# Kernel tuning notes

Hardware: AMD Instinct MI355X
Metric: run time of the kernel (lower is better)

Reference implementation:

```python
import jax, jax.numpy as jnp
import numpy as np

# Dims (match init_kwargs config)
D_L, D_A, D_V = 300, 74, 35
DH_L, DH_A, DH_V = 512, 256, 256
MEM = 512
H_MLP = 1024          # h_att1 = h_att2 = h_gamma1 = h_gamma2 = h_out
T, N = 64, 1024
TOTAL_H = DH_L + DH_A + DH_V          # 1024
ATT_IN = 2 * TOTAL_H                  # 2048 (windowsize=2)
GAMMA_IN = ATT_IN + MEM               # 2560
FINAL = TOTAL_H + MEM                 # 1536


def setup_inputs() -> dict:
    key = jax.random.key(0)
    ks = iter(jax.random.split(key, 64))
    def p(shape):
        return jax.random.normal(next(ks), shape, jnp.float32) * 0.05
    inp = {
        "x": jax.random.normal(next(ks), (T, N, D_L + D_A + D_V), jnp.float32),
        "h_l_prior": jnp.zeros((N, DH_L), jnp.float32),
        "h_a_prior": jnp.zeros((N, DH_A), jnp.float32),
        "h_v_prior": jnp.zeros((N, DH_V), jnp.float32),
        "mem_prior": jnp.zeros((N, MEM), jnp.float32),
        # LSTMCell params (torch layout: W_ih [4H, In], gate order i,f,g,o)
        "W_ih_l": p((4 * DH_L, D_L)), "W_hh_l": p((4 * DH_L, DH_L)),
        "b_ih_l": p((4 * DH_L,)), "b_hh_l": p((4 * DH_L,)),
        "W_ih_a": p((4 * DH_A, D_A)), "W_hh_a": p((4 * DH_A, DH_A)),
        "b_ih_a": p((4 * DH_A,)), "b_hh_a": p((4 * DH_A,)),
        "W_ih_v": p((4 * DH_V, D_V)), "W_hh_v": p((4 * DH_V, DH_V)),
        "b_ih_v": p((4 * DH_V,)), "b_hh_v": p((4 * DH_V,)),
        # attention / gamma / out MLPs (torch Linear: weight [out, in])
        "att1_w1": p((H_MLP, ATT_IN)), "att1_b1": p((H_MLP,)),
        "att1_w2": p((ATT_IN, H_MLP)), "att1_b2": p((ATT_IN,)),
        "att2_w1": p((H_MLP, ATT_IN)), "att2_b1": p((H_MLP,)),
        "att2_w2": p((MEM, H_MLP)), "att2_b2": p((MEM,)),
        "g1_w1": p((H_MLP, GAMMA_IN)), "g1_b1": p((H_MLP,)),
        "g1_w2": p((MEM, H_MLP)), "g1_b2": p((MEM,)),
        "g2_w1": p((H_MLP, GAMMA_IN)), "g2_b1": p((H_MLP,)),
        "g2_w2": p((MEM, H_MLP)), "g2_b2": p((MEM,)),
        "out_w1": p((H_MLP, FINAL)), "out_b1": p((H_MLP,)),
        "out_w2": p((1, H_MLP)), "out_b2": p((1,)),
    }
    return inp


def _lstm_cell(xt, h, c, Wih, Whh, bih, bhh):
    g = xt @ Wih.T + bih + h @ Whh.T + bhh
    i, f, gg, o = jnp.split(g, 4, axis=1)
    c2 = jax.nn.sigmoid(f) * c + jax.nn.sigmoid(i) * jnp.tanh(gg)
    h2 = jax.nn.sigmoid(o) * jnp.tanh(c2)
    return h2, c2


def _mlp2(z, w1, b1, w2, b2):
    # fc2(relu(fc1(z))); dropout is identity at inference
    return jax.nn.relu(z @ w1.T + b1) @ w2.T + b2


def reference(x, h_l_prior, h_a_prior, h_v_prior, mem_prior,
              W_ih_l, W_hh_l, b_ih_l, b_hh_l,
              W_ih_a, W_hh_a, b_ih_a, b_hh_a,
              W_ih_v, W_hh_v, b_ih_v, b_hh_v,
              att1_w1, att1_b1, att1_w2, att1_b2,
              att2_w1, att2_b1, att2_w2, att2_b2,
              g1_w1, g1_b1, g1_w2, g1_b2,
              g2_w1, g2_b1, g2_w2, g2_b2,
              out_w1, out_b1, out_w2, out_b2):
    n = x.shape[1]
    x_l = x[:, :, :D_L]
    x_a = x[:, :, D_L:D_L + D_A]
    x_v = x[:, :, D_L + D_A:]
    # states are re-initialized to zeros (priors unused, as in original forward)
    z = lambda d: jnp.zeros((n, d), x.dtype)
    carry = (z(DH_L), z(DH_L), z(DH_A), z(DH_A), z(DH_V), z(DH_V), z(MEM))

    def step(carry, xs):
        h_l, c_l, h_a, c_a, h_v, c_v, mem = carry
        xl, xa, xv = xs
        nh_l, nc_l = _lstm_cell(xl, h_l, c_l, W_ih_l, W_hh_l, b_ih_l, b_hh_l)
        nh_a, nc_a = _lstm_cell(xa, h_a, c_a, W_ih_a, W_hh_a, b_ih_a, b_hh_a)
        nh_v, nc_v = _lstm_cell(xv, h_v, c_v, W_ih_v, W_hh_v, b_ih_v, b_hh_v)
        # cStar = [prev_cs, new_cs]  -> [n, 2*TOTAL_H]
        cStar = jnp.concatenate([c_l, c_a, c_v, nc_l, nc_a, nc_v], axis=1)
        att = jax.nn.softmax(_mlp2(cStar, att1_w1, att1_b1, att1_w2, att1_b2), axis=1)
        attended = att * cStar
        cHat = jnp.tanh(_mlp2(attended, att2_w1, att2_b1, att2_w2, att2_b2))
        both = jnp.concatenate([attended, mem], axis=1)
        gamma1 = jax.nn.sigmoid(_mlp2(both, g1_w1, g1_b1, g1_w2, g1_b2))
        gamma2 = jax.nn.sigmoid(_mlp2(both, g2_w1, g2_b1, g2_w2, g2_b2))
        mem2 = gamma1 * mem + gamma2 * cHat
        return (nh_l, nc_l, nh_a, nc_a, nh_v, nc_v, mem2), None

    (h_l, c_l, h_a, c_a, h_v, c_v, mem), _ = jax.lax.scan(step, carry, (x_l, x_a, x_v))
    last_hs = jnp.concatenate([h_l, h_a, h_v, mem], axis=1)  # [n, FINAL]
    return _mlp2(last_hs, out_w1, out_b1, out_w2, out_b2)     # [n, 1]
```

## Files before the change

kernel.cpp:

```cpp
#include <hip/hip_runtime.h>
#include <hip/hip_bf16.h>

typedef unsigned short u16;
typedef unsigned int   u32;
typedef __attribute__((ext_vector_type(8))) short s16x8;
typedef __attribute__((ext_vector_type(4))) float f32x4;

#define NB   1024
#define TT   64
#define DXL  300
#define DXA  74
#define DXV  35
#define DX   (DXL+DXA+DXV)
#define DHL  512
#define DHA  256
#define DHV  256
#define TOTH 1024
#define MEMD 512
#define HMLP 1024
#define ATTIN 2048
#define GAMIN 2560
#define PXL  320
#define PXA  128
#define PXV  64

__device__ __forceinline__ u16 f2b(float f) {
    union { float f; u32 u; } x; x.f = f;
    u32 r = x.u + 0x7fffu + ((x.u >> 16) & 1u);
    return (u16)(r >> 16);
}

__device__ __forceinline__ void gload_lds16(const void* g, void* l) {
    __builtin_amdgcn_global_load_lds(
        (const __attribute__((address_space(1))) unsigned int*)g,
        (__attribute__((address_space(3))) unsigned int*)l,
        16, 0, 0);
}

struct GP {
    const u16* A0; const u16* A1; const u16* W0; const u16* W1;
    const float* b0; const float* b1; void* C;
    int lda0, K0, lda1, K1, ldw0, ldw1, ldc, act, outbf, bStart, gx;
};

__global__ __launch_bounds__(256) void gemm_group(GP p0, GP p1, GP p2,
                                                  GP p3, GP p4, GP p5)
{
    __shared__ u16 As[2][64 * 64];
    __shared__ u16 Bs[2][64 * 64];
    GP p;
    {
        int bx = blockIdx.x;
        if      (bx >= p5.bStart) p = p5;
        else if (bx >= p4.bStart) p = p4;
        else if (bx >= p3.bStart) p = p3;
        else if (bx >= p2.bStart) p = p2;
        else if (bx >= p1.bStart) p = p1;
        else                      p = p0;
    }
    const int tid  = threadIdx.x;
    const int wid  = tid >> 6;
    const int lane = tid & 63;
    const int local = blockIdx.x - p.bStart;
    const int by  = local / p.gx;
    const int bm  = by * 64;
    const int bn  = (local - by * p.gx) * 64;
    const int wr = wid >> 1, wc = wid & 1;
    const int nt = (p.K0 + p.K1) >> 6;
    const int e0 = wid * 2 * 64 + lane;

    auto stage = [&](int t, int buf) {
        int k0 = t << 6;
        const u16 *Ap, *Wp; int ldA, ldW, ka;
        if (k0 < p.K0) { Ap = p.A0; ldA = p.lda0; ka = k0;        Wp = p.W0; ldW = p.ldw0; }
        else           { Ap = p.A1; ldA = p.lda1; ka = k0 - p.K0; Wp = p.W1; ldW = p.ldw1; }
        #pragma unroll
        for (int i = 0; i < 2; ++i) {
            int e   = e0 + i * 64;
            int row = e >> 3;
            int c   = (e & 7) ^ (row & 7);
            gload_lds16(Ap + (size_t)(bm + row) * ldA + ka + c * 8,
                        (char*)&As[buf][0] + (wid * 2 + i) * 1024);
            gload_lds16(Wp + (size_t)(bn + row) * ldW + ka + c * 8,
                        (char*)&Bs[buf][0] + (wid * 2 + i) * 1024);
        }
    };

    f32x4 acc[2][2] = {};
    stage(0, 0);
    __syncthreads();

    for (int t = 0; t < nt; ++t) {
        if (t + 1 < nt) stage(t + 1, (t + 1) & 1);
        const char* Ab = (const char*)&As[t & 1][0];
        const char* Bb = (const char*)&Bs[t & 1][0];
        #pragma unroll
        for (int ks = 0; ks < 2; ++ks) {
            s16x8 af[2], bf[2];
            const int ca = ks * 4 + (lane >> 4);
            #pragma unroll
            for (int f = 0; f < 2; ++f) {
                int ra = wr * 32 + f * 16 + (lane & 15);
                af[f] = *(const s16x8*)(Ab + ra * 128 + ((ca ^ (ra & 7))) * 16);
                int rb = wc * 32 + f * 16 + (lane & 15);
                bf[f] = *(const s16x8*)(Bb + rb * 128 + ((ca ^ (rb & 7))) * 16);
            }
            #pragma unroll
            for (int fi = 0; fi < 2; ++fi)
                #pragma unroll
                for (int fj = 0; fj < 2; ++fj)
                    acc[fi][fj] = __builtin_amdgcn_mfma_f32_16x16x32_bf16(
                        af[fi], bf[fj], acc[fi][fj], 0, 0, 0);
        }
        __syncthreads();
    }

    #pragma unroll
    for (int fi = 0; fi < 2; ++fi)
        #pragma unroll
        for (int fj = 0; fj < 2; ++fj) {
            int col = bn + wc * 32 + fj * 16 + (lane & 15);
            float bia = p.b0[col];
            if (p.b1) bia += p.b1[col];
            #pragma unroll
            for (int r4 = 0; r4 < 4; ++r4) {
                int row = bm + wr * 32 + fi * 16 + (lane >> 4) * 4 + r4;
                float v = acc[fi][fj][r4] + bia;
                if (p.act == 1)      v = fmaxf(v, 0.f);
                else if (p.act == 2) v = 1.f / (1.f + __expf(-v));
                else if (p.act == 3) v = tanhf(v);
                if (p.outbf) ((u16*)p.C)[(size_t)row * p.ldc + col] = f2b(v);
                else         ((float*)p.C)[(size_t)row * p.ldc + col] = v;
            }
        }
}

__device__ __forceinline__ void lstm_elem(
    const float* __restrict__ gl, const float* __restrict__ ga,
    const float* __restrict__ gv, const float* __restrict__ cs_prev,
    float* __restrict__ cs_new, u16* __restrict__ cs_new_b,
    u16* __restrict__ hs_new_b, int idx)
{
    int n = idx >> 10, u = idx & 1023;
    const float* g; int dh, gu;
    if (u < DHL)            { g = gl; dh = DHL; gu = u; }
    else if (u < DHL + DHA) { g = ga; dh = DHA; gu = u - DHL; }
    else                    { g = gv; dh = DHV; gu = u - DHL - DHA; }
    const float* grow = g + (size_t)n * 4 * dh;
    float gi = grow[gu], gf = grow[dh + gu], gg = grow[2 * dh + gu], go = grow[3 * dh + gu];
    float c  = cs_prev[idx];
    float si = 1.f / (1.f + __expf(-gi));
    float sf = 1.f / (1.f + __expf(-gf));
    float so = 1.f / (1.f + __expf(-go));
    float c2 = sf * c + si * tanhf(gg);
    float h2 = so * tanhf(c2);
    cs_new[idx]   = c2;
    cs_new_b[idx] = f2b(c2);
    hs_new_b[idx] = f2b(h2);
}

__device__ __forceinline__ void xcvt_elem(
    const float* __restrict__ X, int t, int n, int u,
    u16* __restrict__ xl, u16* __restrict__ xa, u16* __restrict__ xv)
{
    const float* row = X + ((size_t)t * NB + n) * DX;
    if (u < PXL)            xl[n * PXL + u] = f2b(u < DXL ? row[u] : 0.f);
    else if (u < PXL + PXA) { int q = u - PXL;       xa[n * PXA + q] = f2b(q < DXA ? row[DXL + q] : 0.f); }
    else                    { int q = u - PXL - PXA; xv[n * PXV + q] = f2b(q < DXV ? row[DXL + DXA + q] : 0.f); }
}

__global__ void lstm_pointwise(const float* __restrict__ gl,
                               const float* __restrict__ ga,
                               const float* __restrict__ gv,
                               const float* __restrict__ cs_prev,
                               float* __restrict__ cs_new,
                               u16* __restrict__ cs_new_b,
                               u16* __restrict__ hs_new_b,
                               const float* __restrict__ X, int tnext,
                               u16* __restrict__ xl, u16* __restrict__ xa,
                               u16* __restrict__ xv)
{
    int idx = blockIdx.x * blockDim.x + threadIdx.x;
    if (idx >= NB * TOTH) return;
    lstm_elem(gl, ga, gv, cs_prev, cs_new, cs_new_b, hs_new_b, idx);
    int n = idx >> 10, u = idx & 1023;
    if (tnext < TT && u < 512) xcvt_elem(X, tnext, n, u, xl, xa, xv);
}

__global__ __launch_bounds__(256) void fused_mid(
    const float* __restrict__ logits,
    const float* __restrict__ csP,
    const float* __restrict__ csN,
    u16* __restrict__ attended_b,
    int do_mem,
    float* __restrict__ memb, u16* __restrict__ membb,
    const float* __restrict__ g1, const float* __restrict__ g2,
    const float* __restrict__ chat,
    int do_pw,
    const float* __restrict__ gl, const float* __restrict__ ga,
    const float* __restrict__ gv,
    float* __restrict__ pw_cs_new,
    u16* __restrict__ pw_cs_new_b,
    u16* __restrict__ pw_hs_new_b,
    const float* __restrict__ X, int tnext,
    u16* __restrict__ xl, u16* __restrict__ xa, u16* __restrict__ xv)
{
    int n = blockIdx.x;
    int tid = threadIdx.x, lane = tid & 63, wid = tid >> 6;

    if (do_mem) {
        for (int k = tid; k < MEMD; k += 256) {
            size_t i = (size_t)n * MEMD + k;
            float v = g1[i] * memb[i] + g2[i] * chat[i];
            memb[i]  = v;
            membb[i] = f2b(v);
        }
    }

    const float* z = logits + (size_t)n * ATTIN;
    __shared__ float sred[4];

    float m = -1e30f;
    for (int k = tid; k < ATTIN; k += 256) m = fmaxf(m, z[k]);
    #pragma unroll
    for (int off = 1; off < 64; off <<= 1) m = fmaxf(m, __shfl_xor(m, off));
    if (lane == 0) sred[wid] = m;
    __syncthreads();
    m = fmaxf(fmaxf(sred[0], sred[1]), fmaxf(sred[2], sred[3]));
    __syncthreads();

    float s = 0.f;
    for (int k = tid; k < ATTIN; k += 256) s += __expf(z[k] - m);
    #pragma unroll
    for (int off = 1; off < 64; off <<= 1) s += __shfl_xor(s, off);
    if (lane == 0) sred[wid] = s;
    __syncthreads();
    s = sred[0] + sred[1] + sred[2] + sred[3];
    float inv = 1.f / s;

    for (int k = tid; k < ATTIN; k += 256) {
        float cs = (k < TOTH) ? csP[(size_t)n * TOTH + k]
                              : csN[(size_t)n * TOTH + (k - TOTH)];
        attended_b[(size_t)n * ATTIN + k] = f2b(__expf(z[k] - m) * inv * cs);
    }

    if (do_pw) {
        __syncthreads();
        #pragma unroll
        for (int j = 0; j < 4; ++j) {
            int u = tid + j * 256;
            lstm_elem(gl, ga, gv, csN, pw_cs_new, pw_cs_new_b, pw_hs_new_b,
                      n * 1024 + u);
        }
        if (tnext < TT) {
            #pragma unroll
            for (int j = 0; j < 2; ++j) {
                int u = tid + j * 256;
                xcvt_elem(X, tnext, n, u, xl, xa, xv);
            }
        }
    }
}

__global__ void mem_update(float* __restrict__ memb,
                           u16* __restrict__ memb_b,
                           const float* __restrict__ g1,
                           const float* __restrict__ g2,
                           const float* __restrict__ chat)
{
    int idx = blockIdx.x * blockDim.x + threadIdx.x;
    if (idx >= NB * MEMD) return;
    float v = g1[idx] * memb[idx] + g2[idx] * chat[idx];
    memb[idx]   = v;
    memb_b[idx] = f2b(v);
}

__global__ __launch_bounds__(256) void out_dot(const float* __restrict__ hid,
                                               const float* __restrict__ w2,
                                               const float* __restrict__ b2,
                                               float* __restrict__ out)
{
    int wid = threadIdx.x >> 6, lane = threadIdx.x & 63;
    int n = blockIdx.x * 4 + wid;
    if (n >= NB) return;
    const float* h = hid + (size_t)n * HMLP;
    float s = 0.f;
    for (int k = lane; k < HMLP; k += 64) s += h[k] * w2[k];
    #pragma unroll
    for (int off = 1; off < 64; off <<= 1) s += __shfl_xor(s, off);
    if (lane == 0) out[n] = s + b2[0];
}

__global__ void cvt_x(const float* __restrict__ X,
                      u16* __restrict__ xl, u16* __restrict__ xa, u16* __restrict__ xv,
                      int t)
{
    int idx = blockIdx.x * blockDim.x + threadIdx.x;
    if (idx >= NB * 512) return;
    xcvt_elem(X, t, idx >> 9, idx & 511, xl, xa, xv);
}

__global__ void concat2(const float* __restrict__ a, const float* __restrict__ b,
                        float* __restrict__ d)
{
    int i = blockIdx.x * 256 + threadIdx.x;
    if (i < 1024)      d[i] = a[i];
    else if (i < 2048) d[i] = b[i - 1024];
}

#define NWC 15
struct WDesc { const float* src; u16* dst; int rows, ksrc, kdst, bstart; };
struct WPack { WDesc d[NWC]; };

__global__ __launch_bounds__(256) void wcvt_all(WPack wp)
{
    int bx = blockIdx.x;
    int di = 0;
    #pragma unroll
    for (int i = 1; i < NWC; ++i) if (bx >= wp.d[i].bstart) di = i;
    WDesc d = wp.d[di];
    int n = d.rows * d.kdst;
    int base = (bx - d.bstart) * 2048 + threadIdx.x;
    if (d.ksrc == d.kdst) {
        #pragma unroll
        for (int j = 0; j < 8; ++j) {
            int idx = base + j * 256;
            if (idx < n) d.dst[idx] = f2b(d.src[idx]);
        }
    } else {
        #pragma unroll
        for (int j = 0; j < 8; ++j) {
            int idx = base + j * 256;
            if (idx < n) {
                int r = idx / d.kdst, c = idx - r * d.kdst;
                d.dst[idx] = f2b(c < d.ksrc ? d.src[(size_t)r * d.ksrc + c] : 0.f);
            }
        }
    }
}

__global__ void fill0(u32* __restrict__ p, int n)
{
    int i = blockIdx.x * blockDim.x + threadIdx.x;
    if (i < n) p[i] = 0u;
}

static GP mkgp(const u16* A0, int lda0, int K0, const u16* A1, int lda1, int K1,
               const u16* W0, int ldw0, const u16* W1, int ldw1,
               const float* b0, const float* b1, void* C, int ldc,
               int Nout, int act, int outbf)
{
    GP p;
    p.A0 = A0; p.A1 = A1; p.W0 = W0; p.W1 = W1; p.b0 = b0; p.b1 = b1; p.C = C;
    p.lda0 = lda0; p.K0 = K0; p.lda1 = lda1; p.K1 = K1;
    p.ldw0 = ldw0; p.ldw1 = ldw1; p.ldc = ldc; p.act = act; p.outbf = outbf;
    p.bStart = 0; p.gx = Nout / 64;
    return p;
}

static void launch_group(hipStream_t s, GP* p, int np)
{
    int total = 0;
    for (int i = 0; i < np; ++i) { p[i].bStart = total; total += p[i].gx * 16; }
    GP dummy = {};
    dummy.bStart = 0x7fffffff;
    GP a1 = (np > 1) ? p[1] : dummy;
    GP a2 = (np > 2) ? p[2] : dummy;
    GP a3 = (np > 3) ? p[3] : dummy;
    GP a4 = (np > 4) ? p[4] : dummy;
    GP a5 = (np > 5) ? p[5] : dummy;
    gemm_group<<<dim3(total), 256, 0, s>>>(p[0], a1, a2, a3, a4, a5);
}

extern "C" void kernel_launch(void* const* d_in, const int* in_sizes, int n_in,
                              void* d_out, int out_size, void* d_ws, size_t ws_size,
                              hipStream_t stream)
{
    const float* X     = (const float*)d_in[0];
    const float* Wih_l = (const float*)d_in[5];
    const float* Whh_l = (const float*)d_in[6];
    const float* bih_l = (const float*)d_in[7];
    const float* bhh_l = (const float*)d_in[8];
    const float* Wih_a = (const float*)d_in[9];
    const float* Whh_a = (const float*)d_in[10];
    const float* bih_a = (const float*)d_in[11];
    const float* bhh_a = (const float*)d_in[12];
    const float* Wih_v = (const float*)d_in[13];
    const float* Whh_v = (const float*)d_in[14];
    const float* bih_v = (const float*)d_in[15];
    const float* bhh_v = (const float*)d_in[16];
    const float* a1w1  = (const float*)d_in[17];
    const float* a1b1  = (const float*)d_in[18];
    const float* a1w2  = (const float*)d_in[19];
    const float* a1b2  = (const float*)d_in[20];
    const float* a2w1  = (const float*)d_in[21];
    const float* a2b1  = (const float*)d_in[22];
    const float* a2w2  = (const float*)d_in[23];
    const float* a2b2  = (const float*)d_in[24];
    const float* g1w1  = (const float*)d_in[25];
    const float* g1b1  = (const float*)d_in[26];
    const float* g1w2  = (const float*)d_in[27];
    const float* g1b2  = (const float*)d_in[28];
    const float* g2w1  = (const float*)d_in[29];
    const float* g2b1  = (const float*)d_in[30];
    const float* g2w2  = (const float*)d_in[31];
    const float* g2b2  = (const float*)d_in[32];
    const float* ow1   = (const float*)d_in[33];
    const float* ob1   = (const float*)d_in[34];
    const float* ow2   = (const float*)d_in[35];
    const float* ob2   = (const float*)d_in[36];
    float* out = (float*)d_out;

    char* wsp = (char*)d_ws;
    auto take = [&](size_t bytes) -> char* {
        char* r = wsp; wsp += (bytes + 255) & ~(size_t)255; return r;
    };
    float* cs0  = (float*)take((size_t)NB * TOTH * 4);
    float* cs1  = (float*)take((size_t)NB * TOTH * 4);
    float* memb = (float*)take((size_t)NB * MEMD * 4);
    float* gl   = (float*)take((size_t)NB * 2048 * 4);
    float* ga   = (float*)take((size_t)NB * 1024 * 4);
    float* gv   = (float*)take((size_t)NB * 1024 * 4);
    float* lgts = (float*)take((size_t)NB * ATTIN * 4);
    float* chat = (float*)take((size_t)NB * MEMD * 4);
    float* gm1  = (float*)take((size_t)NB * MEMD * 4);
    float* gm2  = (float*)take((size_t)NB * MEMD * 4);
    float* hout = (float*)take((size_t)NB * HMLP * 4);
    float* cb2  = (float*)take((size_t)2048 * 4);
    u16* hs0b  = (u16*)take((size_t)NB * TOTH * 2);
    u16* hs1b  = (u16*)take((size_t)NB * TOTH * 2);
    u16* cs0b  = (u16*)take((size_t)NB * TOTH * 2);
    u16* cs1b  = (u16*)take((size_t)NB * TOTH * 2);
    u16* membb = (u16*)take((size_t)NB * MEMD * 2);
    u16* xlb   = (u16*)take((size_t)NB * PXL * 2);
    u16* xab   = (u16*)take((size_t)NB * PXA * 2);
    u16* xvb   = (u16*)take((size_t)NB * PXV * 2);
    u16* hid1b = (u16*)take((size_t)NB * HMLP * 2);
    u16* hcat  = (u16*)take((size_t)NB * 3072 * 2);
    u16* attdb = (u16*)take((size_t)NB * ATTIN * 2);
    u16* wihlb = (u16*)take((size_t)2048 * PXL * 2);
    u16* whhlb = (u16*)take((size_t)2048 * DHL * 2);
    u16* wihab = (u16*)take((size_t)1024 * PXA * 2);
    u16* whhab = (u16*)take((size_t)1024 * DHA * 2);
    u16* wihvb = (u16*)take((size_t)1024 * PXV * 2);
    u16* whhvb = (u16*)take((size_t)1024 * DHV * 2);
    u16* a1w1b = (u16*)take((size_t)HMLP * ATTIN * 2);
    u16* a1w2b = (u16*)take((size_t)ATTIN * HMLP * 2);
    u16* a2w1b = (u16*)take((size_t)HMLP * ATTIN * 2);
    u16* g12w1b= (u16*)take((size_t)2048 * GAMIN * 2);
    u16* a2w2b = (u16*)take((size_t)MEMD * HMLP * 2);
    u16* g1w2b = (u16*)take((size_t)MEMD * HMLP * 2);
    u16* g2w2b = (u16*)take((size_t)MEMD * HMLP * 2);
    u16* ow1b  = (u16*)take((size_t)HMLP * 1536 * 2);

    {
        int nf = NB * (TOTH * 2 + MEMD);
        fill0<<<(nf + 255) / 256, 256, 0, stream>>>((u32*)cs0, nf);
        int nb = NB * (TOTH * 4 + MEMD) / 2;
        fill0<<<(nb + 255) / 256, 256, 0, stream>>>((u32*)hs0b, nb);
    }
    {
        WPack wp;
        const float* src[NWC] = { Wih_l, Whh_l, Wih_a, Whh_a, Wih_v, Whh_v,
                                  a1w1, a1w2, a2w1, g1w1, g2w1,
                                  a2w2, g1w2, g2w2, ow1 };
        u16* dst[NWC] = { wihlb, whhlb, wihab, whhab, wihvb, whhvb,
                          a1w1b, a1w2b, a2w1b, g12w1b, g12w1b + (size_t)1024 * GAMIN,
                          a2w2b, g1w2b, g2w2b, ow1b };
        int rows[NWC] = { 2048, 2048, 1024, 1024, 1024, 1024,
                          HMLP, ATTIN, HMLP, 1024, 1024,
                          MEMD, MEMD, MEMD, HMLP };
        int ksrc[NWC] = { DXL, DHL, DXA, DHA, DXV, DHV,
                          ATTIN, HMLP, ATTIN, GAMIN, GAMIN,
                          HMLP, HMLP, HMLP, 1536 };
        int kdst[NWC] = { PXL, DHL, PXA, DHA, PXV, DHV,
                          ATTIN, HMLP, ATTIN, GAMIN, GAMIN,
                          HMLP, HMLP, HMLP, 1536 };
        int total = 0;
        for (int i = 0; i < NWC; ++i) {
            wp.d[i].src = src[i]; wp.d[i].dst = dst[i];
            wp.d[i].rows = rows[i]; wp.d[i].ksrc = ksrc[i]; wp.d[i].kdst = kdst[i];
            wp.d[i].bstart = total;
            total += (rows[i] * kdst[i] + 2047) / 2048;
        }
        wcvt_all<<<total, 256, 0, stream>>>(wp);
    }
    concat2<<<8, 256, 0, stream>>>(g1b1, g2b1, cb2);
    cvt_x<<<(NB * 512 + 255) / 256, 256, 0, stream>>>(X, xlb, xab, xvb, 0);

    float* csf[2] = { cs0, cs1 };
    u16*   csb[2] = { cs0b, cs1b };
    u16*   hsb[2] = { hs0b, hs1b };

    {
        GP ps[3] = {
            mkgp(xlb, PXL, PXL, hsb[0], TOTH, DHL,
                 wihlb, PXL, whhlb, DHL, bih_l, bhh_l, gl, 2048, 2048, 0, 0),
            mkgp(xab, PXA, PXA, hsb[0] + DHL, TOTH, DHA,
                 wihab, PXA, whhab, DHA, bih_a, bhh_a, ga, 1024, 1024, 0, 0),
            mkgp(xvb, PXV, PXV, hsb[0] + DHL + DHA, TOTH, DHV,
                 wihvb, PXV, whhvb, DHV, bih_v, bhh_v, gv, 1024, 1024, 0, 0) };
        launch_group(stream, ps, 3);
    }
    lstm_pointwise<<<(NB * TOTH + 255) / 256, 256, 0, stream>>>(
        gl, ga, gv, csf[0], csf[1], csb[1], hsb[1], X, 1, xlb, xab, xvb);
    {
        GP ps[4] = {
            mkgp(csb[0], TOTH, TOTH, csb[1], TOTH, TOTH,
                 a1w1b, ATTIN, a1w1b + TOTH, ATTIN, a1b1, nullptr,
                 hid1b, HMLP, HMLP, 1, 1),
            mkgp(xlb, PXL, PXL, hsb[1], TOTH, DHL,
                 wihlb, PXL, whhlb, DHL, bih_l, bhh_l, gl, 2048, 2048, 0, 0),
            mkgp(xab, PXA, PXA, hsb[1] + DHL, TOTH, DHA,
                 wihab, PXA, whhab, DHA, bih_a, bhh_a, ga, 1024, 1024, 0, 0),
            mkgp(xvb, PXV, PXV, hsb[1] + DHL + DHA, TOTH, DHV,
                 wihvb, PXV, whhvb, DHV, bih_v, bhh_v, gv, 1024, 1024, 0, 0) };
        launch_group(stream, ps, 4);
    }
    {
        GP ps[1] = { mkgp(hid1b, HMLP, HMLP, nullptr, 0, 0,
                          a1w2b, HMLP, nullptr, 0, a1b2, nullptr,
                          lgts, ATTIN, ATTIN, 0, 0) };
        launch_group(stream, ps, 1);
    }

    for (int t = 0; t < TT; ++t) {
        fused_mid<<<NB, 256, 0, stream>>>(
            lgts, csf[t & 1], csf[(t + 1) & 1], attdb,
            t > 0 ? 1 : 0, memb, membb, gm1, gm2, chat,
            t < TT - 1 ? 1 : 0, gl, ga, gv,
            csf[t & 1], csb[t & 1], hsb[t & 1],
            X, t + 2, xlb, xab, xvb);

        {
            GP ps[6]; int np = 0;
            ps[np++] = mkgp(attdb, ATTIN, ATTIN, membb, MEMD, MEMD,
                            g12w1b, GAMIN, g12w1b + ATTIN, GAMIN, cb2, nullptr,
                            hcat + 1024, 3072, 2048, 1, 1);
            ps[np++] = mkgp(attdb, ATTIN, ATTIN, nullptr, 0, 0,
                            a2w1b, ATTIN, nullptr, 0, a2b1, nullptr,
                            hcat, 3072, 1024, 1, 1);
            if (t < TT - 1)
                ps[np++] = mkgp(csb[(t + 1) & 1], TOTH, TOTH, csb[t & 1], TOTH, TOTH,
                                a1w1b, ATTIN, a1w1b + TOTH, ATTIN, a1b1, nullptr,
                                hid1b, HMLP, HMLP, 1, 1);
            if (t < TT - 2) {
                ps[np++] = mkgp(xlb, PXL, PXL, hsb[t & 1], TOTH, DHL,
                                wihlb, PXL, whhlb, DHL, bih_l, bhh_l, gl, 2048, 2048, 0, 0);
                ps[np++] = mkgp(xab, PXA, PXA, hsb[t & 1] + DHL, TOTH, DHA,
                                wihab, PXA, whhab, DHA, bih_a, bhh_a, ga, 1024, 1024, 0, 0);
                ps[np++] = mkgp(xvb, PXV, PXV, hsb[t & 1] + DHL + DHA, TOTH, DHV,
                                wihvb, PXV, whhvb, DHV, bih_v, bhh_v, gv, 1024, 1024, 0, 0);
            }
            launch_group(stream, ps, np);
        }

        {
            GP ps[4]; int np = 0;
            if (t < TT - 1)
                ps[np++] = mkgp(hid1b, HMLP, HMLP, nullptr, 0, 0,
                                a1w2b, HMLP, nullptr, 0, a1b2, nullptr,
                                lgts, ATTIN, ATTIN, 0, 0);
            ps[np++] = mkgp(hcat, 3072, HMLP, nullptr, 0, 0,
                            a2w2b, HMLP, nullptr, 0, a2b2, nullptr, chat, MEMD, MEMD, 3, 0);
            ps[np++] = mkgp(hcat + 1024, 3072, HMLP, nullptr, 0, 0,
                            g1w2b, HMLP, nullptr, 0, g1b2, nullptr, gm1, MEMD, MEMD, 2, 0);
            ps[np++] = mkgp(hcat + 2048, 3072, HMLP, nullptr, 0, 0,
                            g2w2b, HMLP, nullptr, 0, g2b2, nullptr, gm2, MEMD, MEMD, 2, 0);
            launch_group(stream, ps, np);
        }
    }

    mem_update<<<(NB * MEMD + 255) / 256, 256, 0, stream>>>(memb, membb, gm1, gm2, chat);
    {
        GP ps[1] = { mkgp(hsb[0], TOTH, TOTH, membb, MEMD, MEMD,
                          ow1b, 1536, ow1b + TOTH, 1536, ob1, nullptr,
                          hout, HMLP, HMLP, 1, 0) };
        launch_group(stream, ps, 1);
    }
    out_dot<<<NB / 4, 256, 0, stream>>>(hout, ow2, ob2, out);
}
```

Measured before the change: 5.255 ms.

## Prepack weights into MFMA fragment order and load B directly from global

Weights are converted once into a tile- and fragment-major bf16 layout, so each lane reads its B-operand fragment with a single contiguous 16-byte global load. This removes the B shared-memory tile, its async copy and the LDS reads, halving LDS use per block, and launch bounds now request 8 blocks per CU. The cost is that B operands are no longer shared through LDS across waves (each wave fetches its own half from L2/global), and the global load latency sits directly in the MFMA loop with no software prefetch.

```diff
diff --git a/kernel.cpp b/kernel.cpp
--- a/kernel.cpp
+++ b/kernel.cpp
@@ -38,16 +38,15 @@
 }
 
 struct GP {
-    const u16* A0; const u16* A1; const u16* W0; const u16* W1;
+    const u16* A0; const u16* A1; const u16* Wpk;
     const float* b0; const float* b1; void* C;
-    int lda0, K0, lda1, K1, ldw0, ldw1, ldc, act, outbf, bStart, gx;
+    int lda0, K0, lda1, K1, ldc, act, outbf, bStart, gx;
 };
 
-__global__ __launch_bounds__(256) void gemm_group(GP p0, GP p1, GP p2,
-                                                  GP p3, GP p4, GP p5)
+__global__ __launch_bounds__(256, 8) void gemm_group(GP p0, GP p1, GP p2,
+                                                     GP p3, GP p4, GP p5)
 {
     __shared__ u16 As[2][64 * 64];
-    __shared__ u16 Bs[2][64 * 64];
     GP p;
     {
         int bx = blockIdx.x;
@@ -62,18 +61,19 @@
     const int wid  = tid >> 6;
     const int lane = tid & 63;
     const int local = blockIdx.x - p.bStart;
-    const int by  = local / p.gx;
-    const int bm  = by * 64;
-    const int bn  = (local - by * p.gx) * 64;
+    const int by   = local / p.gx;
+    const int bm   = by * 64;
+    const int ntile= local - by * p.gx;
+    const int bn   = ntile * 64;
     const int wr = wid >> 1, wc = wid & 1;
     const int nt = (p.K0 + p.K1) >> 6;
-    const int e0 = wid * 2 * 64 + lane;
-
-    auto stage = [&](int t, int buf) {
+    const int e0 = wid * 128 + lane;
+
+    auto stageA = [&](int t, int buf) {
         int k0 = t << 6;
-        const u16 *Ap, *Wp; int ldA, ldW, ka;
-        if (k0 < p.K0) { Ap = p.A0; ldA = p.lda0; ka = k0;        Wp = p.W0; ldW = p.ldw0; }
-        else           { Ap = p.A1; ldA = p.lda1; ka = k0 - p.K0; Wp = p.W1; ldW = p.ldw1; }
+        const u16* Ap; int ldA, ka;
+        if (k0 < p.K0) { Ap = p.A0; ldA = p.lda0; ka = k0; }
+        else           { Ap = p.A1; ldA = p.lda1; ka = k0 - p.K0; }
         #pragma unroll
         for (int i = 0; i < 2; ++i) {
             int e   = e0 + i * 64;
@@ -81,19 +81,19 @@
             int c   = (e & 7) ^ (row & 7);
             gload_lds16(Ap + (size_t)(bm + row) * ldA + ka + c * 8,
                         (char*)&As[buf][0] + (wid * 2 + i) * 1024);
-            gload_lds16(Wp + (size_t)(bn + row) * ldW + ka + c * 8,
-                        (char*)&Bs[buf][0] + (wid * 2 + i) * 1024);
         }
     };
 
     f32x4 acc[2][2] = {};
-    stage(0, 0);
+    stageA(0, 0);
     __syncthreads();
 
+    const u16* wbase = p.Wpk + ((size_t)ntile * nt << 12) + (wc << 11) + lane * 8;
+
     for (int t = 0; t < nt; ++t) {
-        if (t + 1 < nt) stage(t + 1, (t + 1) & 1);
+        if (t + 1 < nt) stageA(t + 1, (t + 1) & 1);
         const char* Ab = (const char*)&As[t & 1][0];
-        const char* Bb = (const char*)&Bs[t & 1][0];
+        const u16* wt  = wbase + ((size_t)t << 12);
         #pragma unroll
         for (int ks = 0; ks < 2; ++ks) {
             s16x8 af[2], bf[2];
@@ -102,8 +102,7 @@
             for (int f = 0; f < 2; ++f) {
                 int ra = wr * 32 + f * 16 + (lane & 15);
                 af[f] = *(const s16x8*)(Ab + ra * 128 + ((ca ^ (ra & 7))) * 16);
-                int rb = wc * 32 + f * 16 + (lane & 15);
-                bf[f] = *(const s16x8*)(Bb + rb * 128 + ((ca ^ (rb & 7))) * 16);
+                bf[f] = *(const s16x8*)(wt + (ks << 10) + (f << 9));
             }
             #pragma unroll
             for (int fi = 0; fi < 2; ++fi)
@@ -308,34 +307,42 @@
     else if (i < 2048) d[i] = b[i - 1024];
 }
 
-#define NWC 15
-struct WDesc { const float* src; u16* dst; int rows, ksrc, kdst, bstart; };
-struct WPack { WDesc d[NWC]; };
-
-__global__ __launch_bounds__(256) void wcvt_all(WPack wp)
+#define NPK 12
+struct PK {
+    const float* s0; int ld0, k0src, k0;
+    const float* s1; int ld1, k1src;
+    u16* dst; int ntiles, ktot, bstart;
+};
+struct PKPack { PK d[NPK]; };
+
+__global__ __launch_bounds__(256) void wpack_all(PKPack wp)
 {
     int bx = blockIdx.x;
     int di = 0;
     #pragma unroll
-    for (int i = 1; i < NWC; ++i) if (bx >= wp.d[i].bstart) di = i;
-    WDesc d = wp.d[di];
-    int n = d.rows * d.kdst;
-    int base = (bx - d.bstart) * 2048 + threadIdx.x;
-    if (d.ksrc == d.kdst) {
-        #pragma unroll
-        for (int j = 0; j < 8; ++j) {
-            int idx = base + j * 256;
-            if (idx < n) d.dst[idx] = f2b(d.src[idx]);
-        }
-    } else {
-        #pragma unroll
-        for (int j = 0; j < 8; ++j) {
-            int idx = base + j * 256;
-            if (idx < n) {
-                int r = idx / d.kdst, c = idx - r * d.kdst;
-                d.dst[idx] = f2b(c < d.ksrc ? d.src[(size_t)r * d.ksrc + c] : 0.f);
-            }
-        }
+    for (int i = 1; i < NPK; ++i) if (bx >= wp.d[i].bstart) di = i;
+    PK d = wp.d[di];
+    int NT = d.ktot >> 6;
+    int total8 = d.ntiles * 8 * d.ktot;
+    int g = (bx - d.bstart) * 256 + threadIdx.x;
+    if (g >= total8) return;
+    int lane = g & 63;
+    int fj   = (g >> 6) & 1;
+    int ks   = (g >> 7) & 1;
+    int wc   = (g >> 8) & 1;
+    int rest = g >> 9;
+    int t    = rest % NT;
+    int ntile= rest / NT;
+    int row  = ntile * 64 + wc * 32 + fj * 16 + (lane & 15);
+    int kb   = t * 64 + ks * 32 + (lane >> 4) * 8;
+    u16* o = d.dst + (size_t)g * 8;
+    #pragma unroll
+    for (int j = 0; j < 8; ++j) {
+        int k = kb + j;
+        float v;
+        if (k < d.k0) v = (k < d.k0src) ? d.s0[(size_t)row * d.ld0 + k] : 0.f;
+        else { int kk = k - d.k0; v = (kk < d.k1src) ? d.s1[(size_t)row * d.ld1 + kk] : 0.f; }
+        o[j] = f2b(v);
     }
 }
 
@@ -346,14 +353,13 @@
 }
 
 static GP mkgp(const u16* A0, int lda0, int K0, const u16* A1, int lda1, int K1,
-               const u16* W0, int ldw0, const u16* W1, int ldw1,
-               const float* b0, const float* b1, void* C, int ldc,
-               int Nout, int act, int outbf)
+               const u16* Wpk, const float* b0, const float* b1,
+               void* C, int ldc, int Nout, int act, int outbf)
 {
     GP p;
-    p.A0 = A0; p.A1 = A1; p.W0 = W0; p.W1 = W1; p.b0 = b0; p.b1 = b1; p.C = C;
+    p.A0 = A0; p.A1 = A1; p.Wpk = Wpk; p.b0 = b0; p.b1 = b1; p.C = C;
     p.lda0 = lda0; p.K0 = K0; p.lda1 = lda1; p.K1 = K1;
-    p.ldw0 = ldw0; p.ldw1 = ldw1; p.ldc = ldc; p.act = act; p.outbf = outbf;
+    p.ldc = ldc; p.act = act; p.outbf = outbf;
     p.bStart = 0; p.gx = Nout / 64;
     return p;
 }
@@ -438,20 +444,17 @@
     u16* hid1b = (u16*)take((size_t)NB * HMLP * 2);
     u16* hcat  = (u16*)take((size_t)NB * 3072 * 2);
     u16* attdb = (u16*)take((size_t)NB * ATTIN * 2);
-    u16* wihlb = (u16*)take((size_t)2048 * PXL * 2);
-    u16* whhlb = (u16*)take((size_t)2048 * DHL * 2);
-    u16* wihab = (u16*)take((size_t)1024 * PXA * 2);
-    u16* whhab = (u16*)take((size_t)1024 * DHA * 2);
-    u16* wihvb = (u16*)take((size_t)1024 * PXV * 2);
-    u16* whhvb = (u16*)take((size_t)1024 * DHV * 2);
-    u16* a1w1b = (u16*)take((size_t)HMLP * ATTIN * 2);
-    u16* a1w2b = (u16*)take((size_t)ATTIN * HMLP * 2);
-    u16* a2w1b = (u16*)take((size_t)HMLP * ATTIN * 2);
-    u16* g12w1b= (u16*)take((size_t)2048 * GAMIN * 2);
-    u16* a2w2b = (u16*)take((size_t)MEMD * HMLP * 2);
-    u16* g1w2b = (u16*)take((size_t)MEMD * HMLP * 2);
-    u16* g2w2b = (u16*)take((size_t)MEMD * HMLP * 2);
-    u16* ow1b  = (u16*)take((size_t)HMLP * 1536 * 2);
+    u16* lpk    = (u16*)take((size_t)2048 * 832 * 2);
+    u16* apk    = (u16*)take((size_t)1024 * 384 * 2);
+    u16* vpk    = (u16*)take((size_t)1024 * 320 * 2);
+    u16* a1w1pk = (u16*)take((size_t)1024 * 2048 * 2);
+    u16* a1w2pk = (u16*)take((size_t)2048 * 1024 * 2);
+    u16* a2w1pk = (u16*)take((size_t)1024 * 2048 * 2);
+    u16* g12pk  = (u16*)take((size_t)2048 * 2560 * 2);
+    u16* a2w2pk = (u16*)take((size_t)512 * 1024 * 2);
+    u16* g1w2pk = (u16*)take((size_t)512 * 1024 * 2);
+    u16* g2w2pk = (u16*)take((size_t)512 * 1024 * 2);
+    u16* ow1pk  = (u16*)take((size_t)1024 * 1536 * 2);
 
     {
         int nf = NB * (TOTH * 2 + MEMD);
@@ -460,30 +463,29 @@
         fill0<<<(nb + 255) / 256, 256, 0, stream>>>((u32*)hs0b, nb);
     }
     {
-        WPack wp;
-        const float* src[NWC] = { Wih_l, Whh_l, Wih_a, Whh_a, Wih_v, Whh_v,
-                                  a1w1, a1w2, a2w1, g1w1, g2w1,
-                                  a2w2, g1w2, g2w2, ow1 };
-        u16* dst[NWC] = { wihlb, whhlb, wihab, whhab, wihvb, whhvb,
-                          a1w1b, a1w2b, a2w1b, g12w1b, g12w1b + (size_t)1024 * GAMIN,
-                          a2w2b, g1w2b, g2w2b, ow1b };
-        int rows[NWC] = { 2048, 2048, 1024, 1024, 1024, 1024,
-                          HMLP, ATTIN, HMLP, 1024, 1024,
-                          MEMD, MEMD, MEMD, HMLP };
-        int ksrc[NWC] = { DXL, DHL, DXA, DHA, DXV, DHV,
-                          ATTIN, HMLP, ATTIN, GAMIN, GAMIN,
-                          HMLP, HMLP, HMLP, 1536 };
-        int kdst[NWC] = { PXL, DHL, PXA, DHA, PXV, DHV,
-                          ATTIN, HMLP, ATTIN, GAMIN, GAMIN,
-                          HMLP, HMLP, HMLP, 1536 };
+        PKPack wp;
+        PK descs[NPK] = {
+            { Wih_l, DXL, DXL, PXL,  Whh_l, DHL, DHL,  lpk,    32, 832,  0 },
+            { Wih_a, DXA, DXA, PXA,  Whh_a, DHA, DHA,  apk,    16, 384,  0 },
+            { Wih_v, DXV, DXV, PXV,  Whh_v, DHV, DHV,  vpk,    16, 320,  0 },
+            { a1w1, ATTIN, ATTIN, ATTIN, nullptr, 0, 0, a1w1pk, 16, 2048, 0 },
+            { a1w2, HMLP, HMLP, HMLP,    nullptr, 0, 0, a1w2pk, 32, 1024, 0 },
+            { a2w1, ATTIN, ATTIN, ATTIN, nullptr, 0, 0, a2w1pk, 16, 2048, 0 },
+            { g1w1, GAMIN, GAMIN, GAMIN, nullptr, 0, 0, g12pk,  16, 2560, 0 },
+            { g2w1, GAMIN, GAMIN, GAMIN, nullptr, 0, 0, g12pk + (size_t)1024 * 2560, 16, 2560, 0 },
+            { a2w2, HMLP, HMLP, HMLP,    nullptr, 0, 0, a2w2pk,  8, 1024, 0 },
+            { g1w2, HMLP, HMLP, HMLP,    nullptr, 0, 0, g1w2pk,  8, 1024, 0 },
+            { g2w2, HMLP, HMLP, HMLP,    nullptr, 0, 0, g2w2pk,  8, 1024, 0 },
+            { ow1,  1536, 1536, 1536,    nullptr, 0, 0, ow1pk,  16, 1536, 0 },
+        };
         int total = 0;
-        for (int i = 0; i < NWC; ++i) {
-            wp.d[i].src = src[i]; wp.d[i].dst = dst[i];
-            wp.d[i].rows = rows[i]; wp.d[i].ksrc = ksrc[i]; wp.d[i].kdst = kdst[i];
-            wp.d[i].bstart = total;
-            total += (rows[i] * kdst[i] + 2047) / 2048;
-        }
-        wcvt_all<<<total, 256, 0, stream>>>(wp);
+        for (int i = 0; i < NPK; ++i) {
+            descs[i].bstart = total;
+            int groups = descs[i].ntiles * 8 * descs[i].ktot;
+            total += (groups + 255) / 256;
+            wp.d[i] = descs[i];
+        }
+        wpack_all<<<total, 256, 0, stream>>>(wp);
     }
     concat2<<<8, 256, 0, stream>>>(g1b1, g2b1, cb2);
     cvt_x<<<(NB * 512 + 255) / 256, 256, 0, stream>>>(X, xlb, xab, xvb, 0);
@@ -494,32 +496,24 @@
 
     {
         GP ps[3] = {
-            mkgp(xlb, PXL, PXL, hsb[0], TOTH, DHL,
-                 wihlb, PXL, whhlb, DHL, bih_l, bhh_l, gl, 2048, 2048, 0, 0),
-            mkgp(xab, PXA, PXA, hsb[0] + DHL, TOTH, DHA,
-                 wihab, PXA, whhab, DHA, bih_a, bhh_a, ga, 1024, 1024, 0, 0),
-            mkgp(xvb, PXV, PXV, hsb[0] + DHL + DHA, TOTH, DHV,
-                 wihvb, PXV, whhvb, DHV, bih_v, bhh_v, gv, 1024, 1024, 0, 0) };
+            mkgp(xlb, PXL, PXL, hsb[0], TOTH, DHL, lpk, bih_l, bhh_l, gl, 2048, 2048, 0, 0),
+            mkgp(xab, PXA, PXA, hsb[0] + DHL, TOTH, DHA, apk, bih_a, bhh_a, ga, 1024, 1024, 0, 0),
+            mkgp(xvb, PXV, PXV, hsb[0] + DHL + DHA, TOTH, DHV, vpk, bih_v, bhh_v, gv, 1024, 1024, 0, 0) };
         launch_group(stream, ps, 3);
     }
     lstm_pointwise<<<(NB * TOTH + 255) / 256, 256, 0, stream>>>(
         gl, ga, gv, csf[0], csf[1], csb[1], hsb[1], X, 1, xlb, xab, xvb);
     {
         GP ps[4] = {
-            mkgp(csb[0], TOTH, TOTH, csb[1], TOTH, TOTH,
-                 a1w1b, ATTIN, a1w1b + TOTH, ATTIN, a1b1, nullptr,
+            mkgp(csb[0], TOTH, TOTH, csb[1], TOTH, TOTH, a1w1pk, a1b1, nullptr,
                  hid1b, HMLP, HMLP, 1, 1),
-            mkgp(xlb, PXL, PXL, hsb[1], TOTH, DHL,
-                 wihlb, PXL, whhlb, DHL, bih_l, bhh_l, gl, 2048, 2048, 0, 0),
-            mkgp(xab, PXA, PXA, hsb[1] + DHL, TOTH, DHA,
-                 wihab, PXA, whhab, DHA, bih_a, bhh_a, ga, 1024, 1024, 0, 0),
-            mkgp(xvb, PXV, PXV, hsb[1] + DHL + DHA, TOTH, DHV,
-                 wihvb, PXV, whhvb, DHV, bih_v, bhh_v, gv, 1024, 1024, 0, 0) };
+            mkgp(xlb, PXL, PXL, hsb[1], TOTH, DHL, lpk, bih_l, bhh_l, gl, 2048, 2048, 0, 0),
+            mkgp(xab, PXA, PXA, hsb[1] + DHL, TOTH, DHA, apk, bih_a, bhh_a, ga, 1024, 1024, 0, 0),
+            mkgp(xvb, PXV, PXV, hsb[1] + DHL + DHA, TOTH, DHV, vpk, bih_v, bhh_v, gv, 1024, 1024, 0, 0) };
         launch_group(stream, ps, 4);
     }
     {
-        GP ps[1] = { mkgp(hid1b, HMLP, HMLP, nullptr, 0, 0,
-                          a1w2b, HMLP, nullptr, 0, a1b2, nullptr,
+        GP ps[1] = { mkgp(hid1b, HMLP, HMLP, nullptr, 0, 0, a1w2pk, a1b2, nullptr,
                           lgts, ATTIN, ATTIN, 0, 0) };
         launch_group(stream, ps, 1);
     }
@@ -534,23 +528,20 @@
 
         {
             GP ps[6]; int np = 0;
-            ps[np++] = mkgp(attdb, ATTIN, ATTIN, membb, MEMD, MEMD,
-                            g12w1b, GAMIN, g12w1b + ATTIN, GAMIN, cb2, nullptr,
+            ps[np++] = mkgp(attdb, ATTIN, ATTIN, membb, MEMD, MEMD, g12pk, cb2, nullptr,
                             hcat + 1024, 3072, 2048, 1, 1);
-            ps[np++] = mkgp(attdb, ATTIN, ATTIN, nullptr, 0, 0,
-                            a2w1b, ATTIN, nullptr, 0, a2b1, nullptr,
+            ps[np++] = mkgp(attdb, ATTIN, ATTIN, nullptr, 0, 0, a2w1pk, a2b1, nullptr,
                             hcat, 3072, 1024, 1, 1);
             if (t < TT - 1)
                 ps[np++] = mkgp(csb[(t + 1) & 1], TOTH, TOTH, csb[t & 1], TOTH, TOTH,
-                                a1w1b, ATTIN, a1w1b + TOTH, ATTIN, a1b1, nullptr,
-                                hid1b, HMLP, HMLP, 1, 1);
+                                a1w1pk, a1b1, nullptr, hid1b, HMLP, HMLP, 1, 1);
             if (t < TT - 2) {
-                ps[np++] = mkgp(xlb, PXL, PXL, hsb[t & 1], TOTH, DHL,
-                                wihlb, PXL, whhlb, DHL, bih_l, bhh_l, gl, 2048, 2048, 0, 0);
-                ps[np++] = mkgp(xab, PXA, PXA, hsb[t & 1] + DHL, TOTH, DHA,
-                                wihab, PXA, whhab, DHA, bih_a, bhh_a, ga, 1024, 1024, 0, 0);
-                ps[np++] = mkgp(xvb, PXV, PXV, hsb[t & 1] + DHL + DHA, TOTH, DHV,
-                                wihvb, PXV, whhvb, DHV, bih_v, bhh_v, gv, 1024, 1024, 0, 0);
+                ps[np++] = mkgp(xlb, PXL, PXL, hsb[t & 1], TOTH, DHL, lpk,
+                                bih_l, bhh_l, gl, 2048, 2048, 0, 0);
+                ps[np++] = mkgp(xab, PXA, PXA, hsb[t & 1] + DHL, TOTH, DHA, apk,
+                                bih_a, bhh_a, ga, 1024, 1024, 0, 0);
+                ps[np++] = mkgp(xvb, PXV, PXV, hsb[t & 1] + DHL + DHA, TOTH, DHV, vpk,
+                                bih_v, bhh_v, gv, 1024, 1024, 0, 0);
             }
             launch_group(stream, ps, np);
         }
@@ -558,23 +549,21 @@
         {
             GP ps[4]; int np = 0;
             if (t < TT - 1)
-                ps[np++] = mkgp(hid1b, HMLP, HMLP, nullptr, 0, 0,
-                                a1w2b, HMLP, nullptr, 0, a1b2, nullptr,
+                ps[np++] = mkgp(hid1b, HMLP, HMLP, nullptr, 0, 0, a1w2pk, a1b2, nullptr,
                                 lgts, ATTIN, ATTIN, 0, 0);
-            ps[np++] = mkgp(hcat, 3072, HMLP, nullptr, 0, 0,
-                            a2w2b, HMLP, nullptr, 0, a2b2, nullptr, chat, MEMD, MEMD, 3, 0);
-            ps[np++] = mkgp(hcat + 1024, 3072, HMLP, nullptr, 0, 0,
-                            g1w2b, HMLP, nullptr, 0, g1b2, nullptr, gm1, MEMD, MEMD, 2, 0);
-            ps[np++] = mkgp(hcat + 2048, 3072, HMLP, nullptr, 0, 0,
-                            g2w2b, HMLP, nullptr, 0, g2b2, nullptr, gm2, MEMD, MEMD, 2, 0);
+            ps[np++] = mkgp(hcat, 3072, HMLP, nullptr, 0, 0, a2w2pk, a2b2, nullptr,
+                            chat, MEMD, MEMD, 3, 0);
+            ps[np++] = mkgp(hcat + 1024, 3072, HMLP, nullptr, 0, 0, g1w2pk, g1b2, nullptr,
+                            gm1, MEMD, MEMD, 2, 0);
+            ps[np++] = mkgp(hcat + 2048, 3072, HMLP, nullptr, 0, 0, g2w2pk, g2b2, nullptr,
+                            gm2, MEMD, MEMD, 2, 0);
             launch_group(stream, ps, np);
         }
     }
 
     mem_update<<<(NB * MEMD + 255) / 256, 256, 0, stream>>>(memb, membb, gm1, gm2, chat);
     {
-        GP ps[1] = { mkgp(hsb[0], TOTH, TOTH, membb, MEMD, MEMD,
-                          ow1b, 1536, ow1b + TOTH, 1536, ob1, nullptr,
+        GP ps[1] = { mkgp(hsb[0], TOTH, TOTH, membb, MEMD, MEMD, ow1pk, ob1, nullptr,
                           hout, HMLP, HMLP, 1, 0) };
         launch_group(stream, ps, 1);
     }
```

New measurement: 5.424 ms. 1.03x slower.
